# Optimization experiments

Hardware: AMD Instinct MI355X
Metric: run time of the kernel (lower is better)

## Reference

```python
import jax, jax.numpy as jnp
import numpy as np
from jax.scipy.special import gammaln

B, N, K = 16, 65536, 64


def setup_inputs() -> dict:
    key = jax.random.key(0)
    k1, k2, k3, k4, k5 = jax.random.split(key, 5)
    x = jax.random.normal(k1, (B, N), dtype=jnp.float32)
    loc = jnp.full((1,), 0.5, dtype=jnp.float32)          # mean of Normal alpha prior
    scale = jnp.full((1,), -2.0, dtype=jnp.float32)       # softplus(-2) ~ 0.127
    epsilon = jax.random.normal(k3, (1,), dtype=jnp.float32)
    lags = jax.random.randint(k4, (K,), 1, N - 1, dtype=jnp.int64)
    return {"x": x, "loc": loc, "scale": scale, "epsilon": epsilon, "lags": lags}


def _stochastic_frac_deriv(x, alpha, lags):
    """Monte-Carlo Marchaud fractional derivative with k sampled memory lags.

    D^a f(t) ~ a/Gamma(1-a) * (N-1)/k * sum_m (f(t) - f(t - j_m)) * j_m^{-a-1}
    with the term masked out when t < j_m (history does not exist).
    """
    n = x.shape[-1]
    k = lags.shape[0]
    j = jnp.clip(lags, 1, n - 1)                      # [k]
    t = jnp.arange(n)                                 # [N]
    idx = jnp.maximum(t[None, :] - j[:, None], 0)     # [k, N]
    mask = (t[None, :] >= j[:, None]).astype(x.dtype) # [k, N]
    w = j.astype(x.dtype) ** (-(alpha + 1.0))         # kernel weight s^{-a-1}, [k]
    c = alpha * jnp.exp(-gammaln(1.0 - alpha)) * (n - 1) / k  # normalization * MC volume
    xg = x[:, idx]                                    # [B, k, N] gathered history
    contrib = (x[:, None, :] - xg) * (mask * w[:, None])[None, :, :]
    return c * contrib.sum(axis=1)                    # [B, N]


def reference(x, loc, scale, epsilon, lags):
    # reparameterized alpha ~ Normal(loc, softplus(scale))
    alpha = (loc + jax.nn.softplus(scale) * epsilon)[0]
    alpha = jnp.clip(alpha, 0.01, 0.99)               # keep fractional order valid
    return _stochastic_frac_deriv(x, alpha, lags)
```

## Files before the change

kernel.cpp:

```cpp
#include <hip/hip_runtime.h>

#define BB 16
#define NN 65536
#define KK 64
#define TPB 256
#define EPB 1024
#define NBLK ((BB * NN) / EPB)

__device__ __forceinline__ float readlane_f(float v, int lane) {
    return __uint_as_float((unsigned)__builtin_amdgcn_readlane((int)__float_as_uint(v), lane));
}

__device__ __forceinline__ float4 load4(const float* p) {
    float4 v;
    __builtin_memcpy(&v, p, 16);
    return v;
}

__global__ __launch_bounds__(TPB) void frac_deriv_kernel(
    const float* __restrict__ x,
    const float* __restrict__ loc,
    const float* __restrict__ scale,
    const float* __restrict__ eps,
    const int* __restrict__ lags,
    float* __restrict__ out)
{
    __shared__ int   js_raw[KK];
    __shared__ float ws_raw[KK];
    __shared__ int   js[KK];
    __shared__ float ws[KK];

    const int tid  = threadIdx.x;
    const int lane = tid & 63;

    const int bid = blockIdx.x;
    const int swz = (bid & 7) * (NBLK / 8) + (bid >> 3);
    const int b   = swz >> 6;
    const int q   = swz & 63;
    const int T   = q * EPB;

    const float* __restrict__ xr = x + (size_t)b * NN;
    const int e0 = T + 4 * tid;
    const float4 xt = load4(xr + e0);

    if (tid < KK) {
        double s  = (double)scale[0];
        double sp = (s > 20.0) ? s : log1p(exp(s));
        double a  = (double)loc[0] + sp * (double)eps[0];
        a = fmin(fmax(a, 0.01), 0.99);
        double c = a * exp(-lgamma(1.0 - a)) * ((double)(NN - 1) / (double)KK);
        int j = lags[tid];
        j = (j < 1) ? 1 : ((j > NN - 1) ? NN - 1 : j);
        js_raw[tid] = j;
        ws_raw[tid] = (float)(c * exp(-(a + 1.0) * log((double)j)));
    }
    __syncthreads();
    if (tid < KK) {
        const int j = js_raw[tid];
        int rank = 0;
        for (int k = 0; k < KK; ++k) {
            const int jk = js_raw[k];
            rank += (int)((jk < j) || (jk == j && k < tid));
        }
        js[rank] = j;
        ws[rank] = ws_raw[tid];
    }
    __syncthreads();

    const int   jv = js[lane];
    const float wv = ws[lane];
    const int cf = __popcll(__ballot(jv <= T));
    const int cp = __popcll(__ballot(jv <= T + (EPB - 1)));
    const int cf8 = cf & ~7;

    double a0 = 0.0, a1 = 0.0, a2 = 0.0, a3 = 0.0;

    for (int mo = 0; mo < cf8; mo += 8) {
        float4 g = make_float4(0.f, 0.f, 0.f, 0.f);
#pragma unroll
        for (int mi = 0; mi < 8; ++mi) {
            const int   m  = mo + mi;
            const int   jj = __builtin_amdgcn_readlane(jv, m);
            const float w  = readlane_f(wv, m);
            const float4 xg = load4(xr + (e0 - jj));
            g.x = fmaf(xt.x - xg.x, w, g.x);
            g.y = fmaf(xt.y - xg.y, w, g.y);
            g.z = fmaf(xt.z - xg.z, w, g.z);
            g.w = fmaf(xt.w - xg.w, w, g.w);
        }
        a0 += (double)g.x; a1 += (double)g.y; a2 += (double)g.z; a3 += (double)g.w;
    }
    for (int m = cf8; m < cf; ++m) {
        const int   jj = __builtin_amdgcn_readlane(jv, m);
        const float w  = readlane_f(wv, m);
        const float4 xg = load4(xr + (e0 - jj));
        a0 += (double)((xt.x - xg.x) * w);
        a1 += (double)((xt.y - xg.y) * w);
        a2 += (double)((xt.z - xg.z) * w);
        a3 += (double)((xt.w - xg.w) * w);
    }
    for (int m = cf; m < cp; ++m) {
        const int   jj = __builtin_amdgcn_readlane(jv, m);
        const float w  = readlane_f(wv, m);
        const int d0 = e0 - jj;
        const float g0 = xr[(d0     < 0) ? 0 : d0];
        const float g1 = xr[(d0 + 1 < 0) ? 0 : d0 + 1];
        const float g2 = xr[(d0 + 2 < 0) ? 0 : d0 + 2];
        const float g3 = xr[(d0 + 3 < 0) ? 0 : d0 + 3];
        a0 += (d0     >= 0) ? (double)((xt.x - g0) * w) : 0.0;
        a1 += (d0 + 1 >= 0) ? (double)((xt.y - g1) * w) : 0.0;
        a2 += (d0 + 2 >= 0) ? (double)((xt.z - g2) * w) : 0.0;
        a3 += (d0 + 3 >= 0) ? (double)((xt.w - g3) * w) : 0.0;
    }

    float4 r = make_float4((float)a0, (float)a1, (float)a2, (float)a3);
    __builtin_memcpy(out + (size_t)b * NN + e0, &r, 16);
}

extern "C" void kernel_launch(void* const* d_in, const int* in_sizes, int n_in,
                              void* d_out, int out_size, void* d_ws, size_t ws_size,
                              hipStream_t stream) {
    const float* x     = (const float*)d_in[0];
    const float* loc   = (const float*)d_in[1];
    const float* scale = (const float*)d_in[2];
    const float* eps   = (const float*)d_in[3];
    const int*   lags  = (const int*)d_in[4];
    float* out = (float*)d_out;

    frac_deriv_kernel<<<NBLK, TPB, 0, stream>>>(x, loc, scale, eps, lags, out);
}
```

Measured before the change: 16.61 us.

## Double-buffer gathered history loads and reverse block order for heavy-first scheduling

```diff
diff --git a/kernel.cpp b/kernel.cpp
--- a/kernel.cpp
+++ b/kernel.cpp
@@ -11,13 +11,31 @@
     return __uint_as_float((unsigned)__builtin_amdgcn_readlane((int)__float_as_uint(v), lane));
 }
 
-__device__ __forceinline__ float4 load4(const float* p) {
-    float4 v;
-    __builtin_memcpy(&v, p, 16);
-    return v;
-}
+#define LOADG(BUF, BASE)                                                      \
+    do {                                                                      \
+        _Pragma("unroll")                                                     \
+        for (int mi = 0; mi < 8; ++mi) {                                      \
+            const int jj = __builtin_amdgcn_readlane(jv, (BASE) + mi);        \
+            __builtin_memcpy(&BUF[mi], xr + (e0 - jj), 16);                   \
+        }                                                                     \
+    } while (0)
 
-__global__ __launch_bounds__(TPB) void frac_deriv_kernel(
+#define FMAG(BUF, BASE)                                                       \
+    do {                                                                      \
+        float gx = 0.f, gy = 0.f, gz = 0.f, gw = 0.f;                         \
+        _Pragma("unroll")                                                     \
+        for (int mi = 0; mi < 8; ++mi) {                                      \
+            const float wm = readlane_f(wv, (BASE) + mi);                     \
+            gx = fmaf(xt.x - BUF[mi].x, wm, gx);                              \
+            gy = fmaf(xt.y - BUF[mi].y, wm, gy);                              \
+            gz = fmaf(xt.z - BUF[mi].z, wm, gz);                              \
+            gw = fmaf(xt.w - BUF[mi].w, wm, gw);                              \
+        }                                                                     \
+        a0 += (double)gx; a1 += (double)gy;                                   \
+        a2 += (double)gz; a3 += (double)gw;                                   \
+    } while (0)
+
+__global__ __launch_bounds__(TPB, 4) void frac_deriv_kernel(
     const float* __restrict__ x,
     const float* __restrict__ loc,
     const float* __restrict__ scale,
@@ -36,12 +54,13 @@
     const int bid = blockIdx.x;
     const int swz = (bid & 7) * (NBLK / 8) + (bid >> 3);
     const int b   = swz >> 6;
-    const int q   = swz & 63;
+    const int q   = 63 - (swz & 63);
     const int T   = q * EPB;
 
     const float* __restrict__ xr = x + (size_t)b * NN;
     const int e0 = T + 4 * tid;
-    const float4 xt = load4(xr + e0);
+    float4 xt;
+    __builtin_memcpy(&xt, xr + e0, 16);
 
     if (tid < KK) {
         double s  = (double)scale[0];
@@ -71,35 +90,31 @@
     const float wv = ws[lane];
     const int cf = __popcll(__ballot(jv <= T));
     const int cp = __popcll(__ballot(jv <= T + (EPB - 1)));
-    const int cf8 = cf & ~7;
+    const int cf8  = cf & ~7;
+    const int ngrp = cf8 >> 3;
 
     double a0 = 0.0, a1 = 0.0, a2 = 0.0, a3 = 0.0;
 
-    for (int mo = 0; mo < cf8; mo += 8) {
-        float4 g = make_float4(0.f, 0.f, 0.f, 0.f);
-#pragma unroll
-        for (int mi = 0; mi < 8; ++mi) {
-            const int   m  = mo + mi;
-            const int   jj = __builtin_amdgcn_readlane(jv, m);
-            const float w  = readlane_f(wv, m);
-            const float4 xg = load4(xr + (e0 - jj));
-            g.x = fmaf(xt.x - xg.x, w, g.x);
-            g.y = fmaf(xt.y - xg.y, w, g.y);
-            g.z = fmaf(xt.z - xg.z, w, g.z);
-            g.w = fmaf(xt.w - xg.w, w, g.w);
+    float4 A[8], Bv[8];
+    int g = 0;
+    if (ngrp > 0) LOADG(A, 0);
+    for (; g + 2 < ngrp; g += 2) {
+        LOADG(Bv, (g + 1) * 8);
+        FMAG(A, g * 8);
+        LOADG(A, (g + 2) * 8);
+        FMAG(Bv, (g + 1) * 8);
+    }
+    if (g < ngrp) {
+        if (g + 1 < ngrp) {
+            LOADG(Bv, (g + 1) * 8);
+            FMAG(A, g * 8);
+            FMAG(Bv, (g + 1) * 8);
+        } else {
+            FMAG(A, g * 8);
         }
-        a0 += (double)g.x; a1 += (double)g.y; a2 += (double)g.z; a3 += (double)g.w;
     }
-    for (int m = cf8; m < cf; ++m) {
-        const int   jj = __builtin_amdgcn_readlane(jv, m);
-        const float w  = readlane_f(wv, m);
-        const float4 xg = load4(xr + (e0 - jj));
-        a0 += (double)((xt.x - xg.x) * w);
-        a1 += (double)((xt.y - xg.y) * w);
-        a2 += (double)((xt.z - xg.z) * w);
-        a3 += (double)((xt.w - xg.w) * w);
-    }
-    for (int m = cf; m < cp; ++m) {
+
+    for (int m = cf8; m < cp; ++m) {
         const int   jj = __builtin_amdgcn_readlane(jv, m);
         const float w  = readlane_f(wv, m);
         const int d0 = e0 - jj;
```

New measurement: 19.96 us. +20.2%, slower.

## Process two float4 chunks per thread and batch gather loads before FMAs

Applied to the files above, without the earlier changes.

```diff
diff --git a/kernel.cpp b/kernel.cpp
--- a/kernel.cpp
+++ b/kernel.cpp
@@ -4,7 +4,7 @@
 #define NN 65536
 #define KK 64
 #define TPB 256
-#define EPB 1024
+#define EPB 2048
 #define NBLK ((BB * NN) / EPB)
 
 __device__ __forceinline__ float readlane_f(float v, int lane) {
@@ -35,13 +35,15 @@
 
     const int bid = blockIdx.x;
     const int swz = (bid & 7) * (NBLK / 8) + (bid >> 3);
-    const int b   = swz >> 6;
-    const int q   = swz & 63;
+    const int b   = swz >> 5;
+    const int q   = 31 - (swz & 31);
     const int T   = q * EPB;
 
     const float* __restrict__ xr = x + (size_t)b * NN;
     const int e0 = T + 4 * tid;
-    const float4 xt = load4(xr + e0);
+    const int e1 = e0 + 1024;
+    const float4 xt0 = load4(xr + e0);
+    const float4 xt1 = load4(xr + e1);
 
     if (tid < KK) {
         double s  = (double)scale[0];
@@ -74,47 +76,63 @@
     const int cf8 = cf & ~7;
 
     double a0 = 0.0, a1 = 0.0, a2 = 0.0, a3 = 0.0;
+    double a4 = 0.0, a5 = 0.0, a6 = 0.0, a7 = 0.0;
 
     for (int mo = 0; mo < cf8; mo += 8) {
-        float4 g = make_float4(0.f, 0.f, 0.f, 0.f);
+        float4 u[8], v[8];
 #pragma unroll
         for (int mi = 0; mi < 8; ++mi) {
-            const int   m  = mo + mi;
-            const int   jj = __builtin_amdgcn_readlane(jv, m);
-            const float w  = readlane_f(wv, m);
-            const float4 xg = load4(xr + (e0 - jj));
-            g.x = fmaf(xt.x - xg.x, w, g.x);
-            g.y = fmaf(xt.y - xg.y, w, g.y);
-            g.z = fmaf(xt.z - xg.z, w, g.z);
-            g.w = fmaf(xt.w - xg.w, w, g.w);
+            const int jj = __builtin_amdgcn_readlane(jv, mo + mi);
+            const float* bp = xr + (e0 - jj);
+            u[mi] = load4(bp);
+            v[mi] = load4(bp + 1024);
         }
-        a0 += (double)g.x; a1 += (double)g.y; a2 += (double)g.z; a3 += (double)g.w;
-    }
-    for (int m = cf8; m < cf; ++m) {
-        const int   jj = __builtin_amdgcn_readlane(jv, m);
-        const float w  = readlane_f(wv, m);
-        const float4 xg = load4(xr + (e0 - jj));
-        a0 += (double)((xt.x - xg.x) * w);
-        a1 += (double)((xt.y - xg.y) * w);
-        a2 += (double)((xt.z - xg.z) * w);
-        a3 += (double)((xt.w - xg.w) * w);
-    }
-    for (int m = cf; m < cp; ++m) {
-        const int   jj = __builtin_amdgcn_readlane(jv, m);
-        const float w  = readlane_f(wv, m);
-        const int d0 = e0 - jj;
-        const float g0 = xr[(d0     < 0) ? 0 : d0];
-        const float g1 = xr[(d0 + 1 < 0) ? 0 : d0 + 1];
-        const float g2 = xr[(d0 + 2 < 0) ? 0 : d0 + 2];
-        const float g3 = xr[(d0 + 3 < 0) ? 0 : d0 + 3];
-        a0 += (d0     >= 0) ? (double)((xt.x - g0) * w) : 0.0;
-        a1 += (d0 + 1 >= 0) ? (double)((xt.y - g1) * w) : 0.0;
-        a2 += (d0 + 2 >= 0) ? (double)((xt.z - g2) * w) : 0.0;
-        a3 += (d0 + 3 >= 0) ? (double)((xt.w - g3) * w) : 0.0;
+        float g0 = 0.f, g1 = 0.f, g2 = 0.f, g3 = 0.f;
+        float g4 = 0.f, g5 = 0.f, g6 = 0.f, g7 = 0.f;
+#pragma unroll
+        for (int mi = 0; mi < 8; ++mi) {
+            const float wm = readlane_f(wv, mo + mi);
+            g0 = fmaf(xt0.x - u[mi].x, wm, g0);
+            g1 = fmaf(xt0.y - u[mi].y, wm, g1);
+            g2 = fmaf(xt0.z - u[mi].z, wm, g2);
+            g3 = fmaf(xt0.w - u[mi].w, wm, g3);
+            g4 = fmaf(xt1.x - v[mi].x, wm, g4);
+            g5 = fmaf(xt1.y - v[mi].y, wm, g5);
+            g6 = fmaf(xt1.z - v[mi].z, wm, g6);
+            g7 = fmaf(xt1.w - v[mi].w, wm, g7);
+        }
+        a0 += (double)g0; a1 += (double)g1; a2 += (double)g2; a3 += (double)g3;
+        a4 += (double)g4; a5 += (double)g5; a6 += (double)g6; a7 += (double)g7;
     }
 
-    float4 r = make_float4((float)a0, (float)a1, (float)a2, (float)a3);
-    __builtin_memcpy(out + (size_t)b * NN + e0, &r, 16);
+    for (int m = cf8; m < cp; ++m) {
+        const int   jj = __builtin_amdgcn_readlane(jv, m);
+        const float wm = readlane_f(wv, m);
+        const int d0 = e0 - jj;
+        const int d1 = e1 - jj;
+        const float p0 = xr[(d0     < 0) ? 0 : d0];
+        const float p1 = xr[(d0 + 1 < 0) ? 0 : d0 + 1];
+        const float p2 = xr[(d0 + 2 < 0) ? 0 : d0 + 2];
+        const float p3 = xr[(d0 + 3 < 0) ? 0 : d0 + 3];
+        const float p4 = xr[(d1     < 0) ? 0 : d1];
+        const float p5 = xr[(d1 + 1 < 0) ? 0 : d1 + 1];
+        const float p6 = xr[(d1 + 2 < 0) ? 0 : d1 + 2];
+        const float p7 = xr[(d1 + 3 < 0) ? 0 : d1 + 3];
+        a0 += (d0     >= 0) ? (double)((xt0.x - p0) * wm) : 0.0;
+        a1 += (d0 + 1 >= 0) ? (double)((xt0.y - p1) * wm) : 0.0;
+        a2 += (d0 + 2 >= 0) ? (double)((xt0.z - p2) * wm) : 0.0;
+        a3 += (d0 + 3 >= 0) ? (double)((xt0.w - p3) * wm) : 0.0;
+        a4 += (d1     >= 0) ? (double)((xt1.x - p4) * wm) : 0.0;
+        a5 += (d1 + 1 >= 0) ? (double)((xt1.y - p5) * wm) : 0.0;
+        a6 += (d1 + 2 >= 0) ? (double)((xt1.z - p6) * wm) : 0.0;
+        a7 += (d1 + 3 >= 0) ? (double)((xt1.w - p7) * wm) : 0.0;
+    }
+
+    float* __restrict__ orow = out + (size_t)b * NN;
+    float4 r0 = make_float4((float)a0, (float)a1, (float)a2, (float)a3);
+    float4 r1 = make_float4((float)a4, (float)a5, (float)a6, (float)a7);
+    __builtin_memcpy(orow + e0, &r0, 16);
+    __builtin_memcpy(orow + e1, &r1, 16);
 }
 
 extern "C" void kernel_launch(void* const* d_in, const int* in_sizes, int n_in,
```

After: 23.95 us. 44.3% more time.
